# Kernel optimization log

Hardware: AMD Instinct MI355X
Metric: run time of the kernel (lower is better)

The kernel has to match this reference:

```python
import jax, jax.numpy as jnp
import numpy as np

ALPHA = 0.5


def _chamfer(a, b):
    # Equivalent math to cKDTree k=1 queries: exact nearest-neighbor distances
    # between the two flattened clouds, computed brute-force.
    a = a.reshape(-1, 3)
    b = b.reshape(-1, 3)
    d2 = (jnp.sum(a * a, axis=1)[:, None]
          + jnp.sum(b * b, axis=1)[None, :]
          - 2.0 * (a @ b.T))                      # [Na, Nb]
    d = jnp.sqrt(jnp.clip(d2, 0.0))
    dist1 = jnp.min(d, axis=0)   # tree1(a).query(b): NN dist of each b point
    dist2 = jnp.min(d, axis=1)   # tree2(b).query(a): NN dist of each a point
    return jnp.mean(dist1) + jnp.mean(dist2)


def _pairwise_distances(x, y):
    # x: [B,N,3], y: [B,M,3] -> [B,N,M] euclidean distances (clamped-sqrt trick)
    x2 = jnp.sum(x * x, axis=-1, keepdims=True)            # [B,N,1]
    y2 = jnp.sum(y * y, axis=-1, keepdims=True)            # [B,M,1]
    d2 = x2 + jnp.swapaxes(y2, 2, 1) - 2.0 * jnp.einsum('bnd,bmd->bnm', x, y)
    return jnp.sqrt(jnp.clip(d2, 0.0))


def _confidence_scores(input_pcd, gt_pcd):
    # Faithful to torch.norm on the broadcast difference: [B,P,M,3] -> [B,P,M]
    diff = input_pcd[:, :, None, :] - gt_pcd[:, None, :, :]
    dist = jnp.linalg.norm(diff, axis=-1)
    min_d = jnp.min(dist, axis=-1)                         # [B,P]
    return jnp.exp(-min_d)[..., None]                      # [B,P,1]


def setup_inputs() -> dict:
    key = jax.random.key(0)
    k0, k1, k2, k3, k4 = jax.random.split(key, 5)
    B, N, M, P, NS = 4, 2048, 2048, 2048, 1024
    return {
        'pc1_0': jax.random.normal(k0, (B, N, 3), dtype=jnp.float32),
        'pc1_1': jax.random.normal(k1, (B, NS, 3), dtype=jnp.float32),
        'pc1_3': jax.random.uniform(k2, (B, P, 1), dtype=jnp.float32),
        'pc2': jax.random.normal(k3, (B, M, 3), dtype=jnp.float32),
        'pc3': jax.random.normal(k4, (B, P, 3), dtype=jnp.float32),
    }


def reference(pc1_0, pc1_1, pc1_3, pc2, pc3):
    # ChamferDistance detaches inputs in torch (cpu/numpy path) -> stop_gradient
    cd = jax.lax.stop_gradient(_chamfer(pc1_0, pc2))
    # In the original, emd_dist is immediately overwritten by pairwise_distances
    emd_dist = _pairwise_distances(pc1_0, pc2)             # [B,N,M]
    gt_scores = _confidence_scores(pc3, pc2)               # [B,P,1]
    confidence_loss = jnp.mean((pc1_3 - gt_scores) ** 2)
    seed_loss = jax.lax.stop_gradient(_chamfer(pc1_1, pc2))
    upsampling_loss = ALPHA * cd + (1.0 - ALPHA) * emd_dist
    final_loss = confidence_loss + upsampling_loss + seed_loss  # broadcasts to [B,N,M]
    return final_loss
```

## Files before the change

kernel.cpp:

```cpp
#include <hip/hip_runtime.h>
#include <math.h>


constexpr int OUT_TOTAL  = 4 * 2048 * 2048;
constexpr int PART_TOTAL = 832 * 1024;
constexpr int PART_OFS   = OUT_TOTAL - PART_TOTAL;

typedef float nfloat4 __attribute__((ext_vector_type(4)));

__global__ __launch_bounds__(256) void nn_kernel(
    const float* __restrict__ A0,
    const float* __restrict__ A1,
    const float* __restrict__ P2,
    const float* __restrict__ P3,
    float* __restrict__ part)
{
    __shared__ float4 lds[256];
    int bid = blockIdx.x;
    const float* A; const float* Bp; int b_tiles; int local;
    if (bid < 256)      { local = bid;       A = A0; Bp = P2; b_tiles = 32; }
    else if (bid < 512) { local = bid - 256; A = P2; Bp = A0; b_tiles = 32; }
    else if (bid < 640) { local = bid - 512; A = A1; Bp = P2; b_tiles = 32; }
    else if (bid < 768) { local = bid - 640; A = P2; Bp = A1; b_tiles = 16; }
    else { int l2 = bid - 768; int bt = l2 >> 4; local = l2 & 15;
           A = P3 + bt * 6144; Bp = P2 + bt * 6144; b_tiles = 8; }
    int a_tile = local / b_tiles;
    int b_tile = local - a_tile * b_tiles;

    {
        const float* s = Bp + (b_tile * 256 + threadIdx.x) * 3;
        float bx = s[0], by = s[1], bz = s[2];
        float nb2 = -0.5f * fmaf(bx, bx, fmaf(by, by, bz * bz));
        lds[threadIdx.x] = make_float4(bx, by, bz, nb2);
    }

    int a_base = a_tile * 1024 + threadIdx.x * 4;
    const float4* av = (const float4*)(A + a_base * 3);
    float4 v0 = av[0], v1 = av[1], v2 = av[2];
    float ax[4], ay[4], az[4], a2[4], mx[4];
    ax[0]=v0.x; ay[0]=v0.y; az[0]=v0.z;
    ax[1]=v0.w; ay[1]=v1.x; az[1]=v1.y;
    ax[2]=v1.z; ay[2]=v1.w; az[2]=v2.x;
    ax[3]=v2.y; ay[3]=v2.z; az[3]=v2.w;
    #pragma unroll
    for (int k = 0; k < 4; k++) {
        a2[k] = fmaf(ax[k], ax[k], fmaf(ay[k], ay[k], az[k]*az[k]));
        mx[k] = -3.4e38f;
    }
    __syncthreads();

    #pragma unroll 4
    for (int j = 0; j < 256; j++) {
        float4 b = lds[j];
        #pragma unroll
        for (int k = 0; k < 4; k++) {
            float u = fmaf(az[k], b.z, b.w);
            u = fmaf(ay[k], b.y, u);
            u = fmaf(ax[k], b.x, u);
            mx[k] = fmaxf(mx[k], u);
        }
    }
    float4 o;
    o.x = fmaxf(fmaf(-2.f, mx[0], a2[0]), 0.f);
    o.y = fmaxf(fmaf(-2.f, mx[1], a2[1]), 0.f);
    o.z = fmaxf(fmaf(-2.f, mx[2], a2[2]), 0.f);
    o.w = fmaxf(fmaf(-2.f, mx[3], a2[3]), 0.f);
    *(float4*)(part + bid * 1024 + threadIdx.x * 4) = o;
}

__global__ __launch_bounds__(256) void reduce_kernel(
    const float* __restrict__ part,
    const float* __restrict__ conf_in,
    float* __restrict__ ws)
{
    int blk = blockIdx.x;
    int tid = threadIdx.x;
    int pb, bt;
    if (blk < 8)       { pb = blk * 32;              bt = 32; }
    else if (blk < 16) { pb = 256 + (blk - 8) * 32;  bt = 32; }
    else if (blk < 20) { pb = 512 + (blk - 16) * 32; bt = 32; }
    else if (blk < 28) { pb = 640 + (blk - 20) * 16; bt = 16; }
    else               { pb = 768 + (blk - 28) * 8;  bt = 8;  }

    float m0 = 3.4e38f, m1 = 3.4e38f, m2 = 3.4e38f, m3 = 3.4e38f;
    const float* p = part + (pb << 10) + tid;
    #pragma unroll 4
    for (int t = 0; t < bt; t++, p += 1024) {
        m0 = fminf(m0, p[0]);
        m1 = fminf(m1, p[256]);
        m2 = fminf(m2, p[512]);
        m3 = fminf(m3, p[768]);
    }
    float d0 = sqrtf(m0), d1 = sqrtf(m1), d2 = sqrtf(m2), d3 = sqrtf(m3);
    float sum;
    if (blk < 28) {
        sum = (d0 + d1) + (d2 + d3);
    } else {
        const float* c = conf_in + (blk - 28) * 1024 + tid;
        float e0 = c[0]   - __expf(-d0);
        float e1 = c[256] - __expf(-d1);
        float e2 = c[512] - __expf(-d2);
        float e3 = c[768] - __expf(-d3);
        sum = fmaf(e0, e0, e1 * e1) + fmaf(e2, e2, e3 * e3);
    }
    #pragma unroll
    for (int ofs = 32; ofs > 0; ofs >>= 1) sum += __shfl_down(sum, ofs);
    __shared__ float red[4];
    if ((tid & 63) == 0) red[tid >> 6] = sum;
    __syncthreads();
    if (tid == 0) {
        float tot = (red[0] + red[1]) + (red[2] + red[3]);
        float scale = (blk < 16) ? 0.5f / 8192.f
                    : (blk < 20) ? 1.f / 4096.f
                    :              1.f / 8192.f;
        ws[blk] = tot * scale;
    }
}

__global__ __launch_bounds__(256) void out_kernel(
    const float* __restrict__ pc1_0,
    const float* __restrict__ pc2,
    const float* __restrict__ wsp,
    float* __restrict__ out)
{
    int blk = blockIdx.x;
    int batch = blk >> 8;
    int n8 = blk & 255;
    int tid = threadIdx.x;
    float S = 0.f;
    #pragma unroll
    for (int t = 0; t < 36; t++) S += wsp[t];
    const float* bb = pc2 + batch * 6144;
    float bx[8], by[8], bz[8];
    {
        const float4* p = (const float4*)(bb + tid * 12);
        float4 u0 = p[0], u1 = p[1], u2 = p[2];
        bx[0]=u0.x; by[0]=u0.y; bz[0]=u0.z;
        bx[1]=u0.w; by[1]=u1.x; bz[1]=u1.y;
        bx[2]=u1.z; by[2]=u1.w; bz[2]=u2.x;
        bx[3]=u2.y; by[3]=u2.z; bz[3]=u2.w;
    }
    {
        const float4* p = (const float4*)(bb + 3072 + tid * 12);
        float4 u0 = p[0], u1 = p[1], u2 = p[2];
        bx[4]=u0.x; by[4]=u0.y; bz[4]=u0.z;
        bx[5]=u0.w; by[5]=u1.x; bz[5]=u1.y;
        bx[6]=u1.z; by[6]=u1.w; bz[6]=u2.x;
        bx[7]=u2.y; by[7]=u2.z; bz[7]=u2.w;
    }
    const float* arow = pc1_0 + batch * 6144 + n8 * 24;
    float* ob = out + (long)((batch << 11) + (n8 << 3)) * 2048 + tid * 4;
    #pragma unroll
    for (int r = 0; r < 8; r++) {
        float axx = arow[r*3], ayy = arow[r*3+1], azz = arow[r*3+2];
        float o[8];
        #pragma unroll
        for (int k = 0; k < 8; k++) {
            float dx = axx - bx[k], dy = ayy - by[k], dz = azz - bz[k];
            float d2 = fmaf(dx, dx, fmaf(dy, dy, dz*dz));
            o[k] = fmaf(0.5f, sqrtf(d2), S);
        }
        nfloat4 lo = { o[0], o[1], o[2], o[3] };
        nfloat4 hi = { o[4], o[5], o[6], o[7] };
        __builtin_nontemporal_store(lo, (nfloat4*)(ob + r * 2048));
        __builtin_nontemporal_store(hi, (nfloat4*)(ob + r * 2048 + 1024));
    }
}

extern "C" void kernel_launch(void* const* d_in, const int* in_sizes, int n_in,
                              void* d_out, int out_size, void* d_ws, size_t ws_size,
                              hipStream_t stream) {
    const float* pc1_0 = (const float*)d_in[0];
    const float* pc1_1 = (const float*)d_in[1];
    const float* pc1_3 = (const float*)d_in[2];
    const float* pc2   = (const float*)d_in[3];
    const float* pc3   = (const float*)d_in[4];
    float* out = (float*)d_out;
    float* ws  = (float*)d_ws;
    float* part = out + PART_OFS;

    nn_kernel<<<832, 256, 0, stream>>>(pc1_0, pc1_1, pc2, pc3, part);
    reduce_kernel<<<36, 256, 0, stream>>>(part, pc1_3, ws);
    out_kernel<<<1024, 256, 0, stream>>>(pc1_0, pc2, ws, out);
}
```

Measured before the change: 111.5 us.

## Process 8 query points per thread with packed float2 FMA in NN kernel

Each thread in the nearest-neighbour kernel now handles 8 query points instead of 4, so half as many blocks are launched and each LDS load of a reference point is reused across twice as many queries. The inner math uses two-wide vector FMA and max, intended to map to packed FP32 instructions (v_pk_fma_f32). The reduce kernel's indexing is remapped to the new partial-min layout. The cost is more registers per thread and fewer blocks (416) to fill the GPU's compute units.

```diff
diff --git a/kernel.cpp b/kernel.cpp
--- a/kernel.cpp
+++ b/kernel.cpp
@@ -3,10 +3,11 @@
 
 
 constexpr int OUT_TOTAL  = 4 * 2048 * 2048;
-constexpr int PART_TOTAL = 832 * 1024;
+constexpr int PART_TOTAL = 416 * 2048;
 constexpr int PART_OFS   = OUT_TOTAL - PART_TOTAL;
 
 typedef float nfloat4 __attribute__((ext_vector_type(4)));
+typedef float f2 __attribute__((ext_vector_type(2)));
 
 __global__ __launch_bounds__(256) void nn_kernel(
     const float* __restrict__ A0,
@@ -18,11 +19,11 @@
     __shared__ float4 lds[256];
     int bid = blockIdx.x;
     const float* A; const float* Bp; int b_tiles; int local;
-    if (bid < 256)      { local = bid;       A = A0; Bp = P2; b_tiles = 32; }
-    else if (bid < 512) { local = bid - 256; A = P2; Bp = A0; b_tiles = 32; }
-    else if (bid < 640) { local = bid - 512; A = A1; Bp = P2; b_tiles = 32; }
-    else if (bid < 768) { local = bid - 640; A = P2; Bp = A1; b_tiles = 16; }
-    else { int l2 = bid - 768; int bt = l2 >> 4; local = l2 & 15;
+    if (bid < 128)      { local = bid;       A = A0; Bp = P2; b_tiles = 32; }
+    else if (bid < 256) { local = bid - 128; A = P2; Bp = A0; b_tiles = 32; }
+    else if (bid < 320) { local = bid - 256; A = A1; Bp = P2; b_tiles = 32; }
+    else if (bid < 384) { local = bid - 320; A = P2; Bp = A1; b_tiles = 16; }
+    else { int l2 = bid - 384; int bt = l2 >> 3; local = l2 & 7;
            A = P3 + bt * 6144; Bp = P2 + bt * 6144; b_tiles = 8; }
     int a_tile = local / b_tiles;
     int b_tile = local - a_tile * b_tiles;
@@ -34,38 +35,49 @@
         lds[threadIdx.x] = make_float4(bx, by, bz, nb2);
     }
 
-    int a_base = a_tile * 1024 + threadIdx.x * 4;
+    int a_base = a_tile * 2048 + threadIdx.x * 8;
     const float4* av = (const float4*)(A + a_base * 3);
-    float4 v0 = av[0], v1 = av[1], v2 = av[2];
-    float ax[4], ay[4], az[4], a2[4], mx[4];
-    ax[0]=v0.x; ay[0]=v0.y; az[0]=v0.z;
-    ax[1]=v0.w; ay[1]=v1.x; az[1]=v1.y;
-    ax[2]=v1.z; ay[2]=v1.w; az[2]=v2.x;
-    ax[3]=v2.y; ay[3]=v2.z; az[3]=v2.w;
+    float f[24];
     #pragma unroll
-    for (int k = 0; k < 4; k++) {
-        a2[k] = fmaf(ax[k], ax[k], fmaf(ay[k], ay[k], az[k]*az[k]));
-        mx[k] = -3.4e38f;
+    for (int t = 0; t < 6; t++) {
+        float4 q = av[t];
+        f[4*t] = q.x; f[4*t+1] = q.y; f[4*t+2] = q.z; f[4*t+3] = q.w;
+    }
+    f2 ax2[4], ay2[4], az2[4], mx2[4];
+    #pragma unroll
+    for (int p = 0; p < 4; p++) {
+        ax2[p] = (f2){f[6*p+0], f[6*p+3]};
+        ay2[p] = (f2){f[6*p+1], f[6*p+4]};
+        az2[p] = (f2){f[6*p+2], f[6*p+5]};
+        mx2[p] = (f2){-3.4e38f, -3.4e38f};
     }
     __syncthreads();
 
     #pragma unroll 4
     for (int j = 0; j < 256; j++) {
         float4 b = lds[j];
+        f2 bx2 = {b.x, b.x}, by2 = {b.y, b.y}, bz2 = {b.z, b.z}, bw2 = {b.w, b.w};
         #pragma unroll
-        for (int k = 0; k < 4; k++) {
-            float u = fmaf(az[k], b.z, b.w);
-            u = fmaf(ay[k], b.y, u);
-            u = fmaf(ax[k], b.x, u);
-            mx[k] = fmaxf(mx[k], u);
+        for (int p = 0; p < 4; p++) {
+            f2 u = __builtin_elementwise_fma(az2[p], bz2, bw2);
+            u = __builtin_elementwise_fma(ay2[p], by2, u);
+            u = __builtin_elementwise_fma(ax2[p], bx2, u);
+            mx2[p] = __builtin_elementwise_max(mx2[p], u);
         }
     }
-    float4 o;
-    o.x = fmaxf(fmaf(-2.f, mx[0], a2[0]), 0.f);
-    o.y = fmaxf(fmaf(-2.f, mx[1], a2[1]), 0.f);
-    o.z = fmaxf(fmaf(-2.f, mx[2], a2[2]), 0.f);
-    o.w = fmaxf(fmaf(-2.f, mx[3], a2[3]), 0.f);
-    *(float4*)(part + bid * 1024 + threadIdx.x * 4) = o;
+    float o[8];
+    #pragma unroll
+    for (int p = 0; p < 4; p++) {
+        #pragma unroll
+        for (int h = 0; h < 2; h++) {
+            float axx = ax2[p][h], ayy = ay2[p][h], azz = az2[p][h];
+            float a2 = fmaf(axx, axx, fmaf(ayy, ayy, azz * azz));
+            o[2*p+h] = fmaxf(fmaf(-2.f, mx2[p][h], a2), 0.f);
+        }
+    }
+    float* dst = part + bid * 2048 + threadIdx.x * 8;
+    *(float4*)(dst)     = make_float4(o[0], o[1], o[2], o[3]);
+    *(float4*)(dst + 4) = make_float4(o[4], o[5], o[6], o[7]);
 }
 
 __global__ __launch_bounds__(256) void reduce_kernel(
@@ -75,17 +87,17 @@
 {
     int blk = blockIdx.x;
     int tid = threadIdx.x;
-    int pb, bt;
-    if (blk < 8)       { pb = blk * 32;              bt = 32; }
-    else if (blk < 16) { pb = 256 + (blk - 8) * 32;  bt = 32; }
-    else if (blk < 20) { pb = 512 + (blk - 16) * 32; bt = 32; }
-    else if (blk < 28) { pb = 640 + (blk - 20) * 16; bt = 16; }
-    else               { pb = 768 + (blk - 28) * 8;  bt = 8;  }
+    int pbb, bt, ofs;
+    if (blk < 8)       { int l = blk;      pbb = 0   + (l >> 1) * 32; bt = 32; ofs = (l & 1) << 10; }
+    else if (blk < 16) { int l = blk - 8;  pbb = 128 + (l >> 1) * 32; bt = 32; ofs = (l & 1) << 10; }
+    else if (blk < 20) { int l = blk - 16; pbb = 256 + (l >> 1) * 32; bt = 32; ofs = (l & 1) << 10; }
+    else if (blk < 28) { int l = blk - 20; pbb = 320 + (l >> 1) * 16; bt = 16; ofs = (l & 1) << 10; }
+    else               { int l = blk - 28; pbb = 384 + (l >> 1) * 8;  bt = 8;  ofs = (l & 1) << 10; }
 
     float m0 = 3.4e38f, m1 = 3.4e38f, m2 = 3.4e38f, m3 = 3.4e38f;
-    const float* p = part + (pb << 10) + tid;
+    const float* p = part + (pbb << 11) + ofs + tid;
     #pragma unroll 4
-    for (int t = 0; t < bt; t++, p += 1024) {
+    for (int t = 0; t < bt; t++, p += 2048) {
         m0 = fminf(m0, p[0]);
         m1 = fminf(m1, p[256]);
         m2 = fminf(m2, p[512]);
@@ -104,7 +116,7 @@
         sum = fmaf(e0, e0, e1 * e1) + fmaf(e2, e2, e3 * e3);
     }
     #pragma unroll
-    for (int ofs = 32; ofs > 0; ofs >>= 1) sum += __shfl_down(sum, ofs);
+    for (int ofs2 = 32; ofs2 > 0; ofs2 >>= 1) sum += __shfl_down(sum, ofs2);
     __shared__ float red[4];
     if ((tid & 63) == 0) red[tid >> 6] = sum;
     __syncthreads();
@@ -179,7 +191,7 @@
     float* ws  = (float*)d_ws;
     float* part = out + PART_OFS;
 
-    nn_kernel<<<832, 256, 0, stream>>>(pc1_0, pc1_1, pc2, pc3, part);
+    nn_kernel<<<416, 256, 0, stream>>>(pc1_0, pc1_1, pc2, pc3, part);
     reduce_kernel<<<36, 256, 0, stream>>>(part, pc1_3, ws);
     out_kernel<<<1024, 256, 0, stream>>>(pc1_0, pc2, ws, out);
 }
```

Result: no change. 112.3 us (+0.7%).
